# Kernel optimization log

Hardware: AMD Instinct MI355X
Metric: run time of the kernel (lower is better)

The kernel has to match this reference:

```python
import jax, jax.numpy as jnp
import numpy as np

IN_FEATURES = 1024
OUT_FEATURES = 256
GRID_SIZE = 5
SPLINE_ORDER = 3
SCALE_BASE = 1.0
GRID_RANGE = (-1.0, 1.0)


def make_grid():
    h = (GRID_RANGE[1] - GRID_RANGE[0]) / GRID_SIZE
    g = jnp.arange(-SPLINE_ORDER, GRID_SIZE + SPLINE_ORDER + 1, dtype=jnp.float32) * h + GRID_RANGE[0]
    # (in_features, grid_size + 2*spline_order + 1) = (1024, 12)
    return jnp.broadcast_to(g[None, :], (IN_FEATURES, g.shape[0]))


def setup_inputs() -> dict:
    key = jax.random.key(0)
    k1, k2, k3 = jax.random.split(key, 3)
    batch = 16384
    x = jax.random.normal(k1, (batch, IN_FEATURES), dtype=jnp.float32)
    base_weight = jax.random.normal(k2, (OUT_FEATURES, IN_FEATURES), dtype=jnp.float32) * 0.03
    n_basis = GRID_SIZE + SPLINE_ORDER  # 8
    spline_weight = (jax.random.uniform(k3, (OUT_FEATURES, IN_FEATURES * n_basis), dtype=jnp.float32) - 0.5) * 0.1 / n_basis
    grid = make_grid()
    return {"x": x, "base_weight": base_weight, "spline_weight": spline_weight, "grid": grid}


def b_splines(x, grid):
    # x: (B, F) -> (B, F, grid_size + spline_order)
    xe = x[:, :, None]  # (B, F, 1)
    bases = ((xe >= grid[:, :-1]) & (xe < grid[:, 1:])).astype(x.dtype)
    for k in range(1, SPLINE_ORDER + 1):
        left = (xe - grid[:, : -(k + 1)]) / (grid[:, k:-1] - grid[:, : -(k + 1)])
        right = (grid[:, k + 1 :] - xe) / (grid[:, k + 1 :] - grid[:, 1:-k])
        bases = left * bases[:, :, :-1] + right * bases[:, :, 1:]
    return bases.reshape(x.shape[0], -1)  # (B, F*(grid_size+spline_order))


def reference(x, base_weight, spline_weight, grid):
    base_out = jax.nn.silu(x) @ (base_weight * SCALE_BASE).T  # (B, out)
    spline_basis = b_splines(x, grid)                          # (B, F*8)
    spline_out = spline_basis @ spline_weight.T                # (B, out)
    return base_out + spline_out
```

## Files before the change

kernel.cpp:

```cpp
#include <hip/hip_runtime.h>
#include <cstdint>
#include <cstddef>

typedef unsigned short u16;
typedef unsigned int   u32;
typedef unsigned long long u64;
typedef __attribute__((ext_vector_type(8))) short short8;
typedef __attribute__((ext_vector_type(4))) float f32x4;

#define M_ROWS 16384
#define N_COLS 256
#define IN_F   1024
#define K_SPL  8192
#define K_TOT  9216
#define NCHUNK 144
#define SPLITK 2
#define CPB    (NCHUNK / SPLITK)

__device__ __forceinline__ u32 f2bf1(float f) {
  u32 u = __float_as_uint(f);
  u += 0x7fffu + ((u >> 16) & 1u);
  return u >> 16;
}
__device__ __forceinline__ u32 pk2(float a, float b) {
  return f2bf1(a) | (f2bf1(b) << 16);
}
__device__ __forceinline__ float silu(float v) {
  return v * __builtin_amdgcn_rcpf(1.f + __expf(-v));
}

__device__ __forceinline__ uint4 basis8(float xv) {
  float u = fmaf(xv, 2.5f, 5.5f);
  int i0 = (int)u;
  float fr = u - (float)i0;
  float fr2 = fr * fr, fr3 = fr2 * fr;
  float om  = 1.f - fr;
  float om3 = om * om * om;
  float w0 = om3 * (1.f / 6.f);
  float w3 = fr3 * (1.f / 6.f);
  float w1 = fmaf(fr3, 0.5f, fmaf(fr2, -1.f, 2.f / 3.f));
  float w2 = fmaf(fr + fr2 - fr3, 0.5f, 1.f / 6.f);
  u64 W = (u64)pk2(w0, w1) | ((u64)pk2(w2, w3) << 32);
  if (!(u >= 0.f && u < 11.f)) W = 0ull;
  int s = (i0 - 3) * 16;
  u64 lo, hi;
  if (s >= 64)      { int r = s - 64; lo = 0ull; hi = (r < 64) ? (W << r) : 0ull; }
  else if (s > 0)   { lo = W << s;    hi = W >> (64 - s); }
  else if (s == 0)  { lo = W;         hi = 0ull; }
  else              { int r = -s;     lo = (r < 64) ? (W >> r) : 0ull; hi = 0ull; }
  uint4 o;
  o.x = (u32)lo; o.y = (u32)(lo >> 32); o.z = (u32)hi; o.w = (u32)(hi >> 32);
  return o;
}

__global__ void pack_weights(const float* __restrict__ bw, const float* __restrict__ sw,
                             u16* __restrict__ Bp) {
  int o  = blockIdx.y;
  int k4 = (blockIdx.x * blockDim.x + threadIdx.x) * 4;
  const float* src = (k4 < K_SPL) ? (sw + (size_t)o * K_SPL + k4)
                                  : (bw + (size_t)o * IN_F + (k4 - K_SPL));
  float a = src[0], b = src[1], c = src[2], d = src[3];
  uint2 v; v.x = pk2(a, b); v.y = pk2(c, d);
  *(uint2*)(Bp + (size_t)o * K_TOT + k4) = v;
}

__global__ __launch_bounds__(1024, 8)
void kan_gemm(const float* __restrict__ x, const u16* __restrict__ Bp,
              float* __restrict__ out) {
  __shared__ __align__(16) u16 Bs[2 * 256 * 64];
  __shared__ __align__(16) u16 As[2 * 64 * 64];

  const int tid  = threadIdx.x;
  const int lane = tid & 63;
  const int w    = tid >> 6;
  const int wm   = w & 3;
  const int wn   = w >> 2;

  const int bid  = blockIdx.x;
  const int kid  = bid & 1;
  const int mb   = bid >> 1;
  const int row0 = mb * 64;
  const int cs   = kid * CPB, c1 = cs + CPB;

  f32x4 acc[4];
#pragma unroll
  for (int j = 0; j < 4; ++j) acc[j] = (f32x4){0.f, 0.f, 0.f, 0.f};

  const int sr   = (tid >> 3) & 63;
  const int sq   = tid & 7;
  const int bgrp = tid >> 9;

  const int lm = lane & 15;
  const int kg = lane >> 4;
  const int ra = wm * 16 + lm;
  const int a_base = ra * 64 + ((kg ^ (ra & 7)) * 8);
  int b_base[4];
#pragma unroll
  for (int j = 0; j < 4; ++j) {
    int rb = wn * 64 + j * 16 + lm;
    b_base[j] = rb * 64 + ((kg ^ (rb & 7)) * 8);
  }

  u32 stage_goff[2];
  int stage_loff[2];
#pragma unroll
  for (int it = 0; it < 2; ++it) {
    int s  = tid + it * 1024;
    int r_ = s >> 3, cc = (s & 7) ^ (r_ & 7);
    stage_goff[it] = (u32)r_ * K_TOT + cc * 8;
    stage_loff[it] = s * 8;
  }

  float px;
  float4 pb0, pb1;

  auto LOADX = [&](int c) {
    if ((c & 1) != bgrp) return;
    if (c < 128) {
      px = x[(size_t)(row0 + sr) * IN_F + c * 8 + sq];
    } else {
      const float* xp = x + (size_t)(row0 + sr) * IN_F + (c - 128) * 64 + sq * 8;
      pb0 = *(const float4*)xp;
      pb1 = *(const float4*)(xp + 4);
    }
  };

  auto BUILD = [&](int c, int buf) {
    if ((c & 1) != bgrp) return;
    uint4 q;
    if (c < 128) {
      q = basis8(px);
    } else {
      q.x = pk2(silu(pb0.x), silu(pb0.y));
      q.y = pk2(silu(pb0.z), silu(pb0.w));
      q.z = pk2(silu(pb1.x), silu(pb1.y));
      q.w = pk2(silu(pb1.z), silu(pb1.w));
    }
    *(uint4*)(As + buf * (64 * 64) + sr * 64 + ((sq ^ (sr & 7)) * 8)) = q;
  };

  auto STAGEB = [&](int c, int buf) {
    u16* base = Bs + buf * (256 * 64);
#pragma unroll
    for (int it = 0; it < 2; ++it) {
      const u16* gp = Bp + stage_goff[it] + c * 64;
      __builtin_amdgcn_global_load_lds((const __attribute__((address_space(1))) void*)gp,
                                       (__attribute__((address_space(3))) void*)(base + stage_loff[it]),
                                       16, 0, 0);
    }
  };

  auto MFMA_PHASE = [&](int buf) {
    const u16* Ab = As + buf * (64 * 64);
    const u16* Bb = Bs + buf * (256 * 64);
#pragma unroll
    for (int h = 0; h < 2; ++h) {
      const int hx = h * 32;
      short8 af = *(const short8*)(Ab + (a_base ^ hx));
      short8 bf[4];
#pragma unroll
      for (int j = 0; j < 4; ++j) bf[j] = *(const short8*)(Bb + (b_base[j] ^ hx));
#pragma unroll
      for (int j = 0; j < 4; ++j)
        acc[j] = __builtin_amdgcn_mfma_f32_16x16x32_bf16(af, bf[j], acc[j], 0, 0, 0);
    }
  };

  LOADX(cs);
  STAGEB(cs, 0);
  BUILD(cs, 0);
  if (cs + 1 < c1) LOADX(cs + 1);
  __syncthreads();

  for (int c = cs; c < c1; c += 2) {
    if (c + 1 < c1) { STAGEB(c + 1, 1); BUILD(c + 1, 1); }
    if (c + 2 < c1) LOADX(c + 2);
    MFMA_PHASE(0);
    __syncthreads();

    if (c + 1 < c1) {
      if (c + 2 < c1) { STAGEB(c + 2, 0); BUILD(c + 2, 0); }
      if (c + 3 < c1) LOADX(c + 3);
      MFMA_PHASE(1);
      __syncthreads();
    }
  }

  const int lc = lane & 15;
  const int lr = (lane >> 4) * 4;
#pragma unroll
  for (int j = 0; j < 4; ++j) {
    int gr = row0 + wm * 16 + lr;
    int gc = wn * 64 + j * 16 + lc;
    float* po = out + (size_t)gr * N_COLS + gc;
#pragma unroll
    for (int r = 0; r < 4; ++r)
      unsafeAtomicAdd(po + (size_t)r * N_COLS, acc[j][r]);
  }
}

extern "C" void kernel_launch(void* const* d_in, const int* in_sizes, int n_in,
                              void* d_out, int out_size, void* d_ws, size_t ws_size,
                              hipStream_t stream) {
  const float* x  = (const float*)d_in[0];
  const float* bw = (const float*)d_in[1];
  const float* sw = (const float*)d_in[2];
  float* out = (float*)d_out;
  u16* Bp = (u16*)d_ws;

  hipMemsetAsync(d_out, 0, (size_t)M_ROWS * N_COLS * sizeof(float), stream);

  dim3 pgrid(K_TOT / 4 / 256, N_COLS);
  pack_weights<<<pgrid, 256, 0, stream>>>(bw, sw, Bp);

  kan_gemm<<<512, 1024, 0, stream>>>(x, Bp, out);
}
```

Baseline: 204.9 us.

## Split K across waves and give each wave a 32x64 register tile

Waves are rearranged from a 4x4 grid over M and N into a 2x2x4 layout over K-half, M and N. Each wave now computes a 32x64 tile over half of every 64-wide K chunk. Each wave loads 2 A fragments and 4 B fragments from LDS per 8 MFMAs, instead of 10 fragment loads, which cuts LDS read traffic. In exchange, the two K-half waves each atomically add their partial sums to the output, so global atomic traffic doubles, and the accumulator register count doubles.

```diff
diff --git a/kernel.cpp b/kernel.cpp
--- a/kernel.cpp
+++ b/kernel.cpp
@@ -73,7 +73,8 @@
   const int tid  = threadIdx.x;
   const int lane = tid & 63;
   const int w    = tid >> 6;
-  const int wm   = w & 3;
+  const int kh   = w & 1;
+  const int wm   = (w >> 1) & 1;
   const int wn   = w >> 2;
 
   const int bid  = blockIdx.x;
@@ -82,9 +83,12 @@
   const int row0 = mb * 64;
   const int cs   = kid * CPB, c1 = cs + CPB;
 
-  f32x4 acc[4];
-#pragma unroll
-  for (int j = 0; j < 4; ++j) acc[j] = (f32x4){0.f, 0.f, 0.f, 0.f};
+  f32x4 acc[2][4];
+#pragma unroll
+  for (int i = 0; i < 2; ++i)
+#pragma unroll
+    for (int j = 0; j < 4; ++j)
+      acc[i][j] = (f32x4){0.f, 0.f, 0.f, 0.f};
 
   const int sr   = (tid >> 3) & 63;
   const int sq   = tid & 7;
@@ -92,13 +96,17 @@
 
   const int lm = lane & 15;
   const int kg = lane >> 4;
-  const int ra = wm * 16 + lm;
-  const int a_base = ra * 64 + ((kg ^ (ra & 7)) * 8);
-  int b_base[4];
+  const int c4 = kh * 4 + kg;
+  int a_off[2], b_off[4];
+#pragma unroll
+  for (int i = 0; i < 2; ++i) {
+    int ra = wm * 32 + i * 16 + lm;
+    a_off[i] = ra * 64 + ((c4 ^ (ra & 7)) * 8);
+  }
 #pragma unroll
   for (int j = 0; j < 4; ++j) {
     int rb = wn * 64 + j * 16 + lm;
-    b_base[j] = rb * 64 + ((kg ^ (rb & 7)) * 8);
+    b_off[j] = rb * 64 + ((c4 ^ (rb & 7)) * 8);
   }
 
   u32 stage_goff[2];
@@ -153,17 +161,16 @@
   auto MFMA_PHASE = [&](int buf) {
     const u16* Ab = As + buf * (64 * 64);
     const u16* Bb = Bs + buf * (256 * 64);
-#pragma unroll
-    for (int h = 0; h < 2; ++h) {
-      const int hx = h * 32;
-      short8 af = *(const short8*)(Ab + (a_base ^ hx));
-      short8 bf[4];
-#pragma unroll
-      for (int j = 0; j < 4; ++j) bf[j] = *(const short8*)(Bb + (b_base[j] ^ hx));
+    short8 af[2], bf[4];
+#pragma unroll
+    for (int i = 0; i < 2; ++i) af[i] = *(const short8*)(Ab + a_off[i]);
+#pragma unroll
+    for (int j = 0; j < 4; ++j) bf[j] = *(const short8*)(Bb + b_off[j]);
+#pragma unroll
+    for (int i = 0; i < 2; ++i)
 #pragma unroll
       for (int j = 0; j < 4; ++j)
-        acc[j] = __builtin_amdgcn_mfma_f32_16x16x32_bf16(af, bf[j], acc[j], 0, 0, 0);
-    }
+        acc[i][j] = __builtin_amdgcn_mfma_f32_16x16x32_bf16(af[i], bf[j], acc[i][j], 0, 0, 0);
   };
 
   LOADX(cs);
@@ -189,13 +196,16 @@
   const int lc = lane & 15;
   const int lr = (lane >> 4) * 4;
 #pragma unroll
-  for (int j = 0; j < 4; ++j) {
-    int gr = row0 + wm * 16 + lr;
-    int gc = wn * 64 + j * 16 + lc;
-    float* po = out + (size_t)gr * N_COLS + gc;
-#pragma unroll
-    for (int r = 0; r < 4; ++r)
-      unsafeAtomicAdd(po + (size_t)r * N_COLS, acc[j][r]);
+  for (int i = 0; i < 2; ++i) {
+#pragma unroll
+    for (int j = 0; j < 4; ++j) {
+      int gr = row0 + wm * 32 + i * 16 + lr;
+      int gc = wn * 64 + j * 16 + lc;
+      float* po = out + (size_t)gr * N_COLS + gc;
+#pragma unroll
+      for (int r = 0; r < 4; ++r)
+        unsafeAtomicAdd(po + (size_t)r * N_COLS, acc[i][j][r]);
+    }
   }
 }
 
```

Result: slower. 467.6 us (+128.2%).
